# Kernel optimization log

Hardware: AMD Instinct MI355X
Metric: run time of the kernel (lower is better)

Reference implementation:

```python
import jax, jax.numpy as jnp
import numpy as np

H = 8          # num_heads
NB = 2         # block_num
EPS = 1e-8     # LayerNorm eps
NEG = -1e9


def layer_norm(x, g, b):
    m = jnp.mean(x, axis=-1, keepdims=True)
    v = jnp.var(x, axis=-1, keepdims=True)
    return (x - m) / jnp.sqrt(v + EPS) * g + b


def setup_inputs() -> dict:
    key = jax.random.key(0)
    B, L, D = 128, 200, 512
    ks = jax.random.split(key, 24)
    s = 0.02
    inp = {
        'log_seqs': jax.random.randint(ks[0], (B, L), 0, 50),
        'seqs_embs': jax.random.normal(ks[1], (B, L, D), jnp.float32),
        'entire_log_seqs': jax.random.randint(ks[2], (B, L), 0, 50),
        'Wq': jax.random.normal(ks[3], (NB, D, D), jnp.float32) * s,
        'bq': jnp.zeros((NB, D), jnp.float32),
        'Wk': jax.random.normal(ks[4], (NB, D, D), jnp.float32) * s,
        'bk': jnp.zeros((NB, D), jnp.float32),
        'Wv': jax.random.normal(ks[5], (NB, D, D), jnp.float32) * s,
        'bv': jnp.zeros((NB, D), jnp.float32),
        'ln_attn_g': jnp.ones((NB, D), jnp.float32),
        'ln_attn_b': jnp.zeros((NB, D), jnp.float32),
        'ln_fwd_g': jnp.ones((NB, D), jnp.float32),
        'ln_fwd_b': jnp.zeros((NB, D), jnp.float32),
        'W1': jax.random.normal(ks[6], (NB, D, D), jnp.float32) * s,
        'b1': jnp.zeros((NB, D), jnp.float32),
        'W2': jax.random.normal(ks[7], (NB, D, D), jnp.float32) * s,
        'b2': jnp.zeros((NB, D), jnp.float32),
        'ln_last_g': jnp.ones((D,), jnp.float32),
        'ln_last_b': jnp.zeros((D,), jnp.float32),
    }
    return inp


def reference(log_seqs, seqs_embs, entire_log_seqs,
              Wq, bq, Wk, bk, Wv, bv,
              ln_attn_g, ln_attn_b, ln_fwd_g, ln_fwd_b,
              W1, b1, W2, b2, ln_last_g, ln_last_b):
    B, L, D = seqs_embs.shape
    dk = D // H
    scale = 1.0 / np.sqrt(dk).astype(np.float32)

    tl_mask = (log_seqs == 0)            # [B,L] True at target-domain padding (source positions)
    all_mask = (entire_log_seqs != 0)    # [B,L]
    causal = jnp.tril(jnp.ones((L, L), bool))
    # attention_mask = tril * timeline_mask(keys) * all_timeline_mask(keys)
    attn_mask = causal[None, :, :] & tl_mask[:, None, :] & all_mask[:, None, :]  # [B,L,L]
    mf = attn_mask.astype(seqs_embs.dtype)

    keep = (~tl_mask)[..., None].astype(seqs_embs.dtype)  # target positions
    target = seqs_embs * keep
    source = seqs_embs * tl_mask[..., None].astype(seqs_embs.dtype)

    for i in range(NB):
        Qn = layer_norm(target, ln_attn_g[i], ln_attn_b[i])
        q = (Qn @ Wq[i] + bq[i]).reshape(B, L, H, dk).transpose(0, 2, 1, 3)
        k = (source @ Wk[i] + bk[i]).reshape(B, L, H, dk).transpose(0, 2, 1, 3)
        v = (source @ Wv[i] + bv[i]).reshape(B, L, H, dk).transpose(0, 2, 1, 3)
        scores = jnp.einsum('bhqd,bhkd->bhqk', q, k) * scale
        scores = jnp.where(attn_mask[:, None], scores, NEG)
        p = jax.nn.softmax(scores, axis=-1) * mf[:, None]   # double masking
        x = jnp.einsum('bhqk,bhkd->bhqd', p, v)
        x = x.transpose(0, 2, 1, 3).reshape(B, L, D)
        target = x if i == 0 else target + x
        target = layer_norm(target, ln_fwd_g[i], ln_fwd_b[i])
        # PointWiseFeedForward (1x1 convs == per-position linears) + residual
        h = jax.nn.relu(target @ W1[i] + b1[i])
        target = target + (h @ W2[i] + b2[i])
        target = target * keep

    out = layer_norm(target, ln_last_g, ln_last_b) * keep
    return out
```

## Files before the change

### kernel.cpp

```cpp
#include <hip/hip_runtime.h>
#include <hip/hip_bf16.h>

#define BB 128
#define LL 200
#define DD 512
#define HH 8
#define DK 64
#define NBLK 2
#define BL (BB*LL)
#define SCAP 64

typedef unsigned short ushort_t;
typedef unsigned int uint_t;
typedef __attribute__((ext_vector_type(8))) short short8;
typedef __attribute__((ext_vector_type(4))) short short4v;
typedef __attribute__((ext_vector_type(4))) float f32x4;

__device__ inline ushort_t f2b(float x) {
    unsigned u = __float_as_uint(x);
    unsigned r = (u + 0x7FFF + ((u >> 16) & 1)) >> 16;
    return (ushort_t)r;
}

__device__ inline float b2f(ushort_t u) {
    return __uint_as_float((uint_t)u << 16);
}

__device__ inline void gload16(const void* g, void* l) {
    __builtin_amdgcn_global_load_lds((const __attribute__((address_space(1))) void*)g,
                                     (__attribute__((address_space(3))) void*)l,
                                     16, 0, 0);
}

__global__ __launch_bounds__(256) void maskidx_kernel(const int* __restrict__ logs,
                                                      const int* __restrict__ entire,
                                                      float* __restrict__ keepf,
                                                      float* __restrict__ kmf,
                                                      int* __restrict__ kidx,
                                                      int* __restrict__ cntb) {
    int b = blockIdx.x;
    int t = threadIdx.x;
    bool valid = false;
    if (t < LL) {
        int i = b * LL + t;
        bool src = (logs[i] == 0);
        keepf[i] = src ? 0.f : 1.f;
        bool v = src && (entire[i] != 0);
        kmf[i] = v ? 1.f : 0.f;
        valid = v;
    }
    unsigned long long mask = __ballot(valid);
    int wid = t >> 6, lane = t & 63;
    __shared__ int wcnt[4];
    if (lane == 0) wcnt[wid] = __popcll(mask);
    __syncthreads();
    int base = 0;
    for (int k2 = 0; k2 < wid; k2++) base += wcnt[k2];
    int pos = base + __popcll(mask & ((1ull << lane) - 1ull));
    if (valid) kidx[b * LL + pos] = t;
    if (t == 0) cntb[b] = wcnt[0] + wcnt[1] + wcnt[2] + wcnt[3];
}

__global__ __launch_bounds__(128) void scan_kernel(const int* __restrict__ cntb,
                                                   const int* __restrict__ kidx,
                                                   int* __restrict__ off,
                                                   int* __restrict__ rows,
                                                   int* __restrict__ nbk) {
    __shared__ int soff[BB + 1];
    int t = threadIdx.x;
    if (t == 0) {
        int acc = 0;
        for (int b = 0; b < BB; b++) { soff[b] = acc; acc += cntb[b]; }
        soff[BB] = acc;
        nbk[0] = (acc + 127) >> 7;
    }
    __syncthreads();
    int ob = soff[t], nc = cntb[t];
    off[t] = ob;
    for (int s = 0; s < nc; s++)
        rows[ob + s] = t * LL + kidx[t * LL + s];
    __syncthreads();
    if (t == 0) {
        int S = soff[BB];
        int Spad = ((S + 127) >> 7) << 7;
        int last = (S > 0) ? rows[S - 1] : 0;
        for (int s = S; s < Spad; s++) rows[s] = last;
    }
}

__global__ __launch_bounds__(256) void prep_kernel(const int* __restrict__ logs,
                                                   const float* __restrict__ emb,
                                                   float* __restrict__ tgt,
                                                   ushort_t* __restrict__ srcb) {
    int row = blockIdx.x;
    int t = threadIdx.x;
    bool src = (logs[row] == 0);
    float kf = src ? 0.f : 1.f, sf = src ? 1.f : 0.f;
    size_t base = (size_t)row * DD;
    float e0 = emb[base + t], e1 = emb[base + t + 256];
    tgt[base + t] = e0 * kf;
    tgt[base + t + 256] = e1 * kf;
    srcb[base + t] = f2b(e0 * sf);
    srcb[base + t + 256] = f2b(e1 * sf);
}

__global__ __launch_bounds__(256) void wtrans10_kernel(const float* __restrict__ Wq,
                                                       const float* __restrict__ Wk,
                                                       const float* __restrict__ Wv,
                                                       const float* __restrict__ W1,
                                                       const float* __restrict__ W2,
                                                       ushort_t* __restrict__ WqkvT,
                                                       ushort_t* __restrict__ W1T,
                                                       ushort_t* __restrict__ W2T) {
    __shared__ float ts[32][33];
    int tx = threadIdx.x & 31, ty = threadIdx.x >> 5;
    int bx = blockIdx.x * 32, by = blockIdx.y * 32;
    int z = blockIdx.z;
    const float* Wm;
    ushort_t* Wtm;
    if (z < 6) {
        int i = z / 3, j = z - 3 * i;
        const float* src = (j == 0) ? Wq : (j == 1) ? Wk : Wv;
        Wm = src + (size_t)i * DD * DD;
        Wtm = WqkvT + (size_t)z * DD * DD;
    } else if (z < 8) {
        Wm = W1 + (size_t)(z - 6) * DD * DD;
        Wtm = W1T + (size_t)(z - 6) * DD * DD;
    } else {
        Wm = W2 + (size_t)(z - 8) * DD * DD;
        Wtm = W2T + (size_t)(z - 8) * DD * DD;
    }
    #pragma unroll
    for (int i = 0; i < 4; i++) {
        int r = ty + i * 8;
        ts[r][tx] = Wm[(size_t)(by + r) * DD + bx + tx];
    }
    __syncthreads();
    #pragma unroll
    for (int i = 0; i < 4; i++) {
        int r = ty + i * 8;
        Wtm[(size_t)(bx + r) * DD + by + tx] = f2b(ts[tx][r]);
    }
}

__global__ __launch_bounds__(256) void ln_kernel(const float* __restrict__ x,
                                                 const float* __restrict__ addx,
                                                 float* __restrict__ outf,
                                                 ushort_t* __restrict__ outb,
                                                 const float* __restrict__ g,
                                                 const float* __restrict__ bt,
                                                 const float* __restrict__ keepf) {
    int wid = threadIdx.x >> 6, lane = threadIdx.x & 63;
    int row = blockIdx.x * 4 + wid;
    size_t base = (size_t)row * DD;
    int c0 = lane * 4, c1 = c0 + 256;
    f32x4 v0 = *(const f32x4*)(x + base + c0);
    f32x4 v1 = *(const f32x4*)(x + base + c1);
    if (addx) {
        f32x4 a0 = *(const f32x4*)(addx + base + c0);
        f32x4 a1 = *(const f32x4*)(addx + base + c1);
        v0 = v0 + a0;
        v1 = v1 + a1;
    }
    float s = v0[0] + v0[1] + v0[2] + v0[3] + v1[0] + v1[1] + v1[2] + v1[3];
    float sq = v0[0] * v0[0] + v0[1] * v0[1] + v0[2] * v0[2] + v0[3] * v0[3]
             + v1[0] * v1[0] + v1[1] * v1[1] + v1[2] * v1[2] + v1[3] * v1[3];
    #pragma unroll
    for (int off = 32; off; off >>= 1) {
        s += __shfl_xor(s, off);
        sq += __shfl_xor(sq, off);
    }
    float mean = s * (1.f / DD);
    float var = sq * (1.f / DD) - mean * mean;
    float rstd = rsqrtf(fmaxf(var, 0.f) + 1e-8f);
    float kf = keepf ? keepf[row] : 1.f;
    f32x4 g0 = *(const f32x4*)(g + c0), g1 = *(const f32x4*)(g + c1);
    f32x4 b0 = *(const f32x4*)(bt + c0), b1 = *(const f32x4*)(bt + c1);
    f32x4 o0, o1;
    #pragma unroll
    for (int j = 0; j < 4; j++) {
        o0[j] = ((v0[j] - mean) * rstd * g0[j] + b0[j]) * kf;
        o1[j] = ((v1[j] - mean) * rstd * g1[j] + b1[j]) * kf;
    }
    if (outf) {
        *(f32x4*)(outf + base + c0) = o0;
        *(f32x4*)(outf + base + c1) = o1;
    }
    if (outb) {
        short4v ob0, ob1;
        #pragma unroll
        for (int j = 0; j < 4; j++) { ob0[j] = (short)f2b(o0[j]); ob1[j] = (short)f2b(o1[j]); }
        *(short4v*)(outb + base + c0) = ob0;
        *(short4v*)(outb + base + c1) = ob1;
    }
}

__global__ __launch_bounds__(256) void gemm_mfma(const ushort_t* __restrict__ A,
                                                 const ushort_t* __restrict__ Bt,
                                                 const float* __restrict__ bias,
                                                 float* __restrict__ Cf,
                                                 ushort_t* __restrict__ Cb,
                                                 const float* __restrict__ keepf,
                                                 int mode, int M, int N, int K) {
    __shared__ ushort_t smem[12288];
    ushort_t* sAm = smem;
    ushort_t* sBm = smem + 4096;
    int t = threadIdx.x;
    int w = t >> 6, lane = t & 63;
    int lr = lane & 15, lq = lane >> 4;

    int nwg = (M >> 6) * (N >> 7);
    int cpx = nwg >> 3;
    int swz = (blockIdx.x & 7) * cpx + (blockIdx.x >> 3);
    int m0 = (swz >> 2) * 64;
    int n0 = (swz & 3) * 128;

    f32x4 acc[4][2] = {};

    int eA = t * 8, rowA = eA >> 5, colA = eA & 31;

    for (int k0 = 0; k0 < K; k0 += 64) {
        #pragma unroll
        for (int hh = 0; hh < 2; hh++) {
            gload16(A + (size_t)(m0 + rowA) * K + k0 + hh * 32 + colA,
                    sAm + hh * 2048 + (w * 64) * 8);
            #pragma unroll
            for (int r = 0; r < 2; r++) {
                int e = (r * 256 + t) * 8;
                int row = e >> 5, col = e & 31;
                gload16(Bt + (size_t)(n0 + row) * K + k0 + hh * 32 + col,
                        sBm + hh * 4096 + (r * 256 + w * 64) * 8);
            }
        }
        __syncthreads();

        #pragma unroll
        for (int hh = 0; hh < 2; hh++) {
            short8 af[4], bf[2];
            #pragma unroll
            for (int mt = 0; mt < 4; mt++)
                af[mt] = *(const short8*)(sAm + hh * 2048 + (mt * 16 + lr) * 32 + lq * 8);
            #pragma unroll
            for (int nt = 0; nt < 2; nt++)
                bf[nt] = *(const short8*)(sBm + hh * 4096 + (w * 32 + nt * 16 + lr) * 32 + lq * 8);
            #pragma unroll
            for (int mt = 0; mt < 4; mt++)
                #pragma unroll
                for (int nt = 0; nt < 2; nt++)
                    acc[mt][nt] = __builtin_amdgcn_mfma_f32_16x16x32_bf16(af[mt], bf[nt], acc[mt][nt], 0, 0, 0);
        }
        __syncthreads();
    }

    if (mode != 2) {
        #pragma unroll
        for (int nt = 0; nt < 2; nt++) {
            int colL = w * 32 + nt * 16 + lr;
            float bv = bias[n0 + colL];
            #pragma unroll
            for (int mt = 0; mt < 4; mt++) {
                int rowL = mt * 16 + lq * 4;
                #pragma unroll
                for (int r = 0; r < 4; r++) {
                    float o = acc[mt][nt][r] + bv;
                    if (mode == 1) o = fmaxf(o, 0.f);
                    smem[(rowL + r) * 136 + colL] = f2b(o);
                }
            }
        }
        __syncthreads();
        int rr = t >> 2, cc = (t & 3) * 32;
        #pragma unroll
        for (int j = 0; j < 4; j++) {
            short8 vv = *(const short8*)(smem + rr * 136 + cc + j * 8);
            *(short8*)(Cb + (size_t)(m0 + rr) * N + n0 + cc + j * 8) = vv;
        }
    } else {
        float* sf = (float*)smem;
        #pragma unroll
        for (int half = 0; half < 2; half++) {
            #pragma unroll
            for (int nt = 0; nt < 2; nt++) {
                int colL = w * 32 + nt * 16 + lr;
                float bv = bias[n0 + colL];
                #pragma unroll
                for (int mt = half * 2; mt < half * 2 + 2; mt++) {
                    int rowL = mt * 16 + lq * 4 - half * 32;
                    #pragma unroll
                    for (int r = 0; r < 4; r++)
                        sf[(rowL + r) * 132 + colL] = acc[mt][nt][r] + bv;
                }
            }
            __syncthreads();
            int rr = t >> 3, cc = (t & 7) * 16;
            int grow = m0 + half * 32 + rr;
            float kf = keepf[grow];
            #pragma unroll
            for (int j = 0; j < 4; j++) {
                f32x4 oldv = *(const f32x4*)(Cf + (size_t)grow * N + n0 + cc + j * 4);
                f32x4 nv;
                #pragma unroll
                for (int x = 0; x < 4; x++)
                    nv[x] = (oldv[x] + sf[rr * 132 + cc + j * 4 + x]) * kf;
                *(f32x4*)(Cf + (size_t)grow * N + n0 + cc + j * 4) = nv;
            }
            __syncthreads();
        }
    }
}

__global__ __launch_bounds__(256) void gemm_kv(const ushort_t* __restrict__ A,
                                               const ushort_t* __restrict__ Bqkv,
                                               const float* __restrict__ bk,
                                               const float* __restrict__ bv,
                                               const int* __restrict__ rows,
                                               const int* __restrict__ nbk,
                                               ushort_t* __restrict__ kc,
                                               ushort_t* __restrict__ vc) {
    __shared__ ushort_t sA[2][128 * 32];
    __shared__ ushort_t sB[2][128 * 32];
    int z = blockIdx.z;
    const ushort_t* Bt = Bqkv + (size_t)(1 + z) * DD * DD;
    const float* bias = z ? bv : bk;
    ushort_t* C = z ? vc : kc;

    int t = threadIdx.x;
    int w = t >> 6, lane = t & 63;
    int wm = w & 1, wn = w >> 1;
    int n0 = blockIdx.y * 128;
    int lr = lane & 15, lq = lane >> 4;
    int colA = (t & 3) * 8;
    int nb = nbk[0];

    for (int mb = blockIdx.x; mb < nb; mb += gridDim.x) {
        int m0 = mb * 128;
        int ra0 = rows[m0 + (t >> 2)];
        int ra1 = rows[m0 + 64 + (t >> 2)];

        f32x4 acc[4][4] = {};

        for (int k0 = 0; k0 < DD; k0 += 64) {
            #pragma unroll
            for (int hh = 0; hh < 2; hh++) {
                gload16(A + (size_t)ra0 * DD + k0 + hh * 32 + colA,
                        sA[hh] + (0 * 256 + w * 64) * 8);
                gload16(A + (size_t)ra1 * DD + k0 + hh * 32 + colA,
                        sA[hh] + (1 * 256 + w * 64) * 8);
                #pragma unroll
                for (int r = 0; r < 2; r++) {
                    int e = (r * 256 + t) * 8;
                    int row = e >> 5, col = e & 31;
                    gload16(Bt + (size_t)(n0 + row) * DD + k0 + hh * 32 + col,
                            sB[hh] + (r * 256 + w * 64) * 8);
                }
            }
            __syncthreads();

            #pragma unroll
            for (int hh = 0; hh < 2; hh++) {
                short8 af[4], bf[4];
                #pragma unroll
                for (int mt = 0; mt < 4; mt++)
                    af[mt] = *(const short8*)(sA[hh] + (wm * 64 + mt * 16 + lr) * 32 + lq * 8);
                #pragma unroll
                for (int nt = 0; nt < 4; nt++)
                    bf[nt] = *(const short8*)(sB[hh] + (wn * 64 + nt * 16 + lr) * 32 + lq * 8);
                #pragma unroll
                for (int mt = 0; mt < 4; mt++)
                    #pragma unroll
                    for (int nt = 0; nt < 4; nt++)
                        acc[mt][nt] = __builtin_amdgcn_mfma_f32_16x16x32_bf16(af[mt], bf[nt], acc[mt][nt], 0, 0, 0);
            }
            __syncthreads();
        }

        #pragma unroll
        for (int nt = 0; nt < 4; nt++) {
            int col = n0 + wn * 64 + nt * 16 + lr;
            float bv2 = bias[col];
            #pragma unroll
            for (int mt = 0; mt < 4; mt++) {
                int rowb = m0 + wm * 64 + mt * 16 + lq * 4;
                #pragma unroll
                for (int r = 0; r < 4; r++)
                    C[(size_t)(rowb + r) * DD + col] = f2b(acc[mt][nt][r] + bv2);
            }
        }
    }
}

__global__ __launch_bounds__(256) void attn_sparse(const ushort_t* __restrict__ q,
                                                   const ushort_t* __restrict__ kc,
                                                   const ushort_t* __restrict__ vc,
                                                   const int* __restrict__ kidx,
                                                   const int* __restrict__ cntb,
                                                   const int* __restrict__ off,
                                                   float* __restrict__ xout) {
    __shared__ ushort_t sK[SCAP * DK];
    __shared__ ushort_t sV[SCAP * DK];
    __shared__ int sIdx[LL];
    int b = blockIdx.x >> 3, h = blockIdx.x & 7;
    int t = threadIdx.x;
    int w = t >> 6, lane = t & 63;
    int qi = lane >> 3;
    int dc = (lane & 7) * 8;
    int nc = cntb[b], ob = off[b];
    const ushort_t* qg = q + (size_t)b * LL * DD + h * DK;
    float* og = xout + (size_t)b * LL * DD + h * DK;
    const ushort_t* kb2 = kc + (size_t)ob * DD + h * DK;
    const ushort_t* vb2 = vc + (size_t)ob * DD + h * DK;

    if (t < nc) sIdx[t] = kidx[b * LL + t];
    int ns = (nc < SCAP) ? nc : SCAP;
    for (int idx = t; idx < ns * 8; idx += 256) {
        int s = idx >> 3, c = (idx & 7) * 8;
        *(uint4*)(sK + s * DK + c) = *(const uint4*)(kb2 + (size_t)s * DD + c);
        *(uint4*)(sV + s * DK + c) = *(const uint4*)(vb2 + (size_t)s * DD + c);
    }
    __syncthreads();

    for (int i0 = 0; i0 < LL; i0 += 32) {
        int i = i0 + w * 8 + qi;
        bool qok = (i < LL);
        int ic = qok ? i : (LL - 1);
        short8 qv = *(const short8*)(qg + (size_t)ic * DD + dc);
        float qf[8];
        #pragma unroll
        for (int j = 0; j < 8; j++) qf[j] = b2f((ushort_t)qv[j]);

        float m = -3.0e38f, l = 0.f;
        float acc[8];
        #pragma unroll
        for (int j = 0; j < 8; j++) acc[j] = 0.f;

        for (int s = 0; s < nc; s++) {
            const ushort_t* kp = (s < SCAP) ? (sK + s * DK + dc)
                                            : (kb2 + (size_t)s * DD + dc);
            const ushort_t* vp = (s < SCAP) ? (sV + s * DK + dc)
                                            : (vb2 + (size_t)s * DD + dc);
            short8 k8 = *(const short8*)kp;
            float pp = 0.f;
            #pragma unroll
            for (int j = 0; j < 8; j++) pp += qf[j] * b2f((ushort_t)k8[j]);
            pp += __shfl_xor(pp, 1);
            pp += __shfl_xor(pp, 2);
            pp += __shfl_xor(pp, 4);
            bool ok = (sIdx[s] <= i);
            float sc = ok ? pp * 0.125f : -3.0e38f;
            float mn = fmaxf(m, sc);
            float e = ok ? __expf(sc - mn) : 0.f;
            float rs2 = __expf(m - mn);
            l = l * rs2 + e;
            short8 v8 = *(const short8*)vp;
            #pragma unroll
            for (int j = 0; j < 8; j++)
                acc[j] = acc[j] * rs2 + e * b2f((ushort_t)v8[j]);
            m = mn;
        }

        if (qok) {
            float inv = (l > 0.f) ? 1.f / l : 0.f;
            f32x4 o0, o1;
            #pragma unroll
            for (int j = 0; j < 4; j++) { o0[j] = acc[j] * inv; o1[j] = acc[j + 4] * inv; }
            *(f32x4*)(og + (size_t)i * DD + dc) = o0;
            *(f32x4*)(og + (size_t)i * DD + dc + 4) = o1;
        }
    }
}

extern "C" void kernel_launch(void* const* d_in, const int* in_sizes, int n_in,
                              void* d_out, int out_size, void* d_ws, size_t ws_size,
                              hipStream_t stream) {
    const int* log_seqs = (const int*)d_in[0];
    const float* seqs_embs = (const float*)d_in[1];
    const int* entire = (const int*)d_in[2];
    const float* Wq = (const float*)d_in[3];
    const float* bq = (const float*)d_in[4];
    const float* Wk = (const float*)d_in[5];
    const float* bk = (const float*)d_in[6];
    const float* Wv = (const float*)d_in[7];
    const float* bv = (const float*)d_in[8];
    const float* lag = (const float*)d_in[9];
    const float* lab = (const float*)d_in[10];
    const float* lfg = (const float*)d_in[11];
    const float* lfb = (const float*)d_in[12];
    const float* W1 = (const float*)d_in[13];
    const float* b1 = (const float*)d_in[14];
    const float* W2 = (const float*)d_in[15];
    const float* b2 = (const float*)d_in[16];
    const float* llg = (const float*)d_in[17];
    const float* llb = (const float*)d_in[18];
    float* out = (float*)d_out;
    float* ws = (float*)d_ws;

    const size_t n = (size_t)BL * DD;
    float* tgt = ws;
    float* aout = ws + n;
    ushort_t* srcb = (ushort_t*)(ws + 2 * n);
    ushort_t* qb = srcb + n;
    ushort_t* kc = qb + n;
    ushort_t* lnb = kc + n;
    ushort_t* WqkvT = lnb + n;
    ushort_t* W1T = WqkvT + (size_t)NBLK * 3 * DD * DD;
    ushort_t* W2T = W1T + (size_t)NBLK * DD * DD;
    float* keepf = (float*)(W2T + (size_t)NBLK * DD * DD);
    float* kmf = keepf + BL;
    ushort_t* vc = (ushort_t*)(kmf + BL);
    int* kidx = (int*)(vc + n);
    int* cntb = kidx + BL;
    int* offb = cntb + BB;
    int* rows = offb + BB;
    int* nbk = rows + BL + 128;
    ushort_t* hb = qb;

    maskidx_kernel<<<BB, 256, 0, stream>>>(log_seqs, entire, keepf, kmf, kidx, cntb);
    scan_kernel<<<1, 128, 0, stream>>>(cntb, kidx, offb, rows, nbk);
    prep_kernel<<<BL, 256, 0, stream>>>(log_seqs, seqs_embs, tgt, srcb);
    dim3 tw(16, 16, 10);
    wtrans10_kernel<<<tw, 256, 0, stream>>>(Wq, Wk, Wv, W1, W2, WqkvT, W1T, W2T);

    int ngg = (BL / 64) * (DD / 128);
    int nln = BL / 4;
    dim3 gkv(32, DD / 128, 2);
    for (int i = 0; i < NBLK; i++) {
        size_t wo = (size_t)i * DD * DD;
        gemm_kv<<<gkv, 256, 0, stream>>>(srcb, WqkvT + (size_t)i * 3 * DD * DD,
                                         bk + i * DD, bv + i * DD, rows, nbk, kc, vc);
        ln_kernel<<<nln, 256, 0, stream>>>(tgt, nullptr, nullptr, lnb,
                                           lag + i * DD, lab + i * DD, nullptr);
        gemm_mfma<<<ngg, 256, 0, stream>>>(lnb, WqkvT + (size_t)i * 3 * DD * DD,
                                           bq + i * DD, nullptr, qb, nullptr,
                                           0, BL, DD, DD);
        attn_sparse<<<BB * HH, 256, 0, stream>>>(qb, kc, vc, kidx, cntb, offb, aout);
        ln_kernel<<<nln, 256, 0, stream>>>(aout, (i == 0) ? nullptr : tgt, tgt, lnb,
                                           lfg + i * DD, lfb + i * DD, nullptr);
        gemm_mfma<<<ngg, 256, 0, stream>>>(lnb, W1T + wo, b1 + i * DD, nullptr, hb,
                                           nullptr, 1, BL, DD, DD);
        gemm_mfma<<<ngg, 256, 0, stream>>>(hb, W2T + wo, b2 + i * DD, tgt, nullptr,
                                           keepf, 2, BL, DD, DD);
    }
    ln_kernel<<<nln, 256, 0, stream>>>(tgt, nullptr, out, nullptr, llg, llb, keepf);
}
```

Measured before the change: 531.6 us.

## Merge sparse K/V projection into Q GEMM launch and vectorize prep kernel

The separate gather-based K/V GEMM kernel is removed. Its work is now done by 64 extra workgroups appended to the Q-projection GEMM launch, each looping over 64-row tiles of the compacted source rows with the same 64x128 tile code. This removes one launch per block and lets the K/V work overlap the Q GEMM, but changes the K/V tile shape from 128x128 to 64x128 and limits that part to 64 workgroups, which could become the tail. Separately, the prep kernel now handles four rows per block with vector loads and stores.

```diff
diff --git a/kernel.cpp b/kernel.cpp
--- a/kernel.cpp
+++ b/kernel.cpp
@@ -92,16 +92,27 @@
                                                    const float* __restrict__ emb,
                                                    float* __restrict__ tgt,
                                                    ushort_t* __restrict__ srcb) {
-    int row = blockIdx.x;
-    int t = threadIdx.x;
+    int wid = threadIdx.x >> 6, lane = threadIdx.x & 63;
+    int row = blockIdx.x * 4 + wid;
     bool src = (logs[row] == 0);
     float kf = src ? 0.f : 1.f, sf = src ? 1.f : 0.f;
     size_t base = (size_t)row * DD;
-    float e0 = emb[base + t], e1 = emb[base + t + 256];
-    tgt[base + t] = e0 * kf;
-    tgt[base + t + 256] = e1 * kf;
-    srcb[base + t] = f2b(e0 * sf);
-    srcb[base + t + 256] = f2b(e1 * sf);
+    int c0 = lane * 4, c1 = c0 + 256;
+    f32x4 e0 = *(const f32x4*)(emb + base + c0);
+    f32x4 e1 = *(const f32x4*)(emb + base + c1);
+    f32x4 t0, t1;
+    short4v s0, s1;
+    #pragma unroll
+    for (int j = 0; j < 4; j++) {
+        t0[j] = e0[j] * kf;
+        t1[j] = e1[j] * kf;
+        s0[j] = (short)f2b(e0[j] * sf);
+        s1[j] = (short)f2b(e1[j] * sf);
+    }
+    *(f32x4*)(tgt + base + c0) = t0;
+    *(f32x4*)(tgt + base + c1) = t1;
+    *(short4v*)(srcb + base + c0) = s0;
+    *(short4v*)(srcb + base + c1) = s1;
 }
 
 __global__ __launch_bounds__(256) void wtrans10_kernel(const float* __restrict__ Wq,
@@ -201,190 +212,188 @@
                                                  float* __restrict__ Cf,
                                                  ushort_t* __restrict__ Cb,
                                                  const float* __restrict__ keepf,
-                                                 int mode, int M, int N, int K) {
+                                                 int mode, int M, int N, int K, int ngg,
+                                                 const ushort_t* __restrict__ Akv,
+                                                 const ushort_t* __restrict__ Bkv,
+                                                 const float* __restrict__ bk,
+                                                 const float* __restrict__ bv,
+                                                 const int* __restrict__ rows,
+                                                 const int* __restrict__ nbk,
+                                                 ushort_t* __restrict__ kc,
+                                                 ushort_t* __restrict__ vc) {
     __shared__ ushort_t smem[12288];
     ushort_t* sAm = smem;
     ushort_t* sBm = smem + 4096;
     int t = threadIdx.x;
     int w = t >> 6, lane = t & 63;
     int lr = lane & 15, lq = lane >> 4;
-
-    int nwg = (M >> 6) * (N >> 7);
-    int cpx = nwg >> 3;
-    int swz = (blockIdx.x & 7) * cpx + (blockIdx.x >> 3);
-    int m0 = (swz >> 2) * 64;
-    int n0 = (swz & 3) * 128;
-
-    f32x4 acc[4][2] = {};
-
     int eA = t * 8, rowA = eA >> 5, colA = eA & 31;
 
-    for (int k0 = 0; k0 < K; k0 += 64) {
-        #pragma unroll
-        for (int hh = 0; hh < 2; hh++) {
-            gload16(A + (size_t)(m0 + rowA) * K + k0 + hh * 32 + colA,
-                    sAm + hh * 2048 + (w * 64) * 8);
-            #pragma unroll
-            for (int r = 0; r < 2; r++) {
-                int e = (r * 256 + t) * 8;
-                int row = e >> 5, col = e & 31;
-                gload16(Bt + (size_t)(n0 + row) * K + k0 + hh * 32 + col,
-                        sBm + hh * 4096 + (r * 256 + w * 64) * 8);
-            }
-        }
-        __syncthreads();
-
-        #pragma unroll
-        for (int hh = 0; hh < 2; hh++) {
-            short8 af[4], bf[2];
-            #pragma unroll
-            for (int mt = 0; mt < 4; mt++)
-                af[mt] = *(const short8*)(sAm + hh * 2048 + (mt * 16 + lr) * 32 + lq * 8);
-            #pragma unroll
-            for (int nt = 0; nt < 2; nt++)
-                bf[nt] = *(const short8*)(sBm + hh * 4096 + (w * 32 + nt * 16 + lr) * 32 + lq * 8);
-            #pragma unroll
-            for (int mt = 0; mt < 4; mt++)
-                #pragma unroll
-                for (int nt = 0; nt < 2; nt++)
-                    acc[mt][nt] = __builtin_amdgcn_mfma_f32_16x16x32_bf16(af[mt], bf[nt], acc[mt][nt], 0, 0, 0);
-        }
-        __syncthreads();
-    }
-
-    if (mode != 2) {
-        #pragma unroll
-        for (int nt = 0; nt < 2; nt++) {
-            int colL = w * 32 + nt * 16 + lr;
-            float bv = bias[n0 + colL];
-            #pragma unroll
-            for (int mt = 0; mt < 4; mt++) {
-                int rowL = mt * 16 + lq * 4;
-                #pragma unroll
-                for (int r = 0; r < 4; r++) {
-                    float o = acc[mt][nt][r] + bv;
-                    if (mode == 1) o = fmaxf(o, 0.f);
-                    smem[(rowL + r) * 136 + colL] = f2b(o);
-                }
-            }
-        }
-        __syncthreads();
-        int rr = t >> 2, cc = (t & 3) * 32;
-        #pragma unroll
-        for (int j = 0; j < 4; j++) {
-            short8 vv = *(const short8*)(smem + rr * 136 + cc + j * 8);
-            *(short8*)(Cb + (size_t)(m0 + rr) * N + n0 + cc + j * 8) = vv;
-        }
-    } else {
-        float* sf = (float*)smem;
-        #pragma unroll
-        for (int half = 0; half < 2; half++) {
-            #pragma unroll
-            for (int nt = 0; nt < 2; nt++) {
-                int colL = w * 32 + nt * 16 + lr;
-                float bv = bias[n0 + colL];
-                #pragma unroll
-                for (int mt = half * 2; mt < half * 2 + 2; mt++) {
-                    int rowL = mt * 16 + lq * 4 - half * 32;
-                    #pragma unroll
-                    for (int r = 0; r < 4; r++)
-                        sf[(rowL + r) * 132 + colL] = acc[mt][nt][r] + bv;
-                }
-            }
-            __syncthreads();
-            int rr = t >> 3, cc = (t & 7) * 16;
-            int grow = m0 + half * 32 + rr;
-            float kf = keepf[grow];
-            #pragma unroll
-            for (int j = 0; j < 4; j++) {
-                f32x4 oldv = *(const f32x4*)(Cf + (size_t)grow * N + n0 + cc + j * 4);
-                f32x4 nv;
-                #pragma unroll
-                for (int x = 0; x < 4; x++)
-                    nv[x] = (oldv[x] + sf[rr * 132 + cc + j * 4 + x]) * kf;
-                *(f32x4*)(Cf + (size_t)grow * N + n0 + cc + j * 4) = nv;
-            }
-            __syncthreads();
-        }
-    }
-}
-
-__global__ __launch_bounds__(256) void gemm_kv(const ushort_t* __restrict__ A,
-                                               const ushort_t* __restrict__ Bqkv,
-                                               const float* __restrict__ bk,
-                                               const float* __restrict__ bv,
-                                               const int* __restrict__ rows,
-                                               const int* __restrict__ nbk,
-                                               ushort_t* __restrict__ kc,
-                                               ushort_t* __restrict__ vc) {
-    __shared__ ushort_t sA[2][128 * 32];
-    __shared__ ushort_t sB[2][128 * 32];
-    int z = blockIdx.z;
-    const ushort_t* Bt = Bqkv + (size_t)(1 + z) * DD * DD;
-    const float* bias = z ? bv : bk;
-    ushort_t* C = z ? vc : kc;
-
-    int t = threadIdx.x;
-    int w = t >> 6, lane = t & 63;
-    int wm = w & 1, wn = w >> 1;
-    int n0 = blockIdx.y * 128;
-    int lr = lane & 15, lq = lane >> 4;
-    int colA = (t & 3) * 8;
-    int nb = nbk[0];
-
-    for (int mb = blockIdx.x; mb < nb; mb += gridDim.x) {
-        int m0 = mb * 128;
-        int ra0 = rows[m0 + (t >> 2)];
-        int ra1 = rows[m0 + 64 + (t >> 2)];
-
-        f32x4 acc[4][4] = {};
-
-        for (int k0 = 0; k0 < DD; k0 += 64) {
+    if ((int)blockIdx.x < ngg) {
+        int cpx = ngg >> 3;
+        int swz = (blockIdx.x & 7) * cpx + (blockIdx.x >> 3);
+        int m0 = (swz >> 2) * 64;
+        int n0 = (swz & 3) * 128;
+
+        f32x4 acc[4][2] = {};
+
+        for (int k0 = 0; k0 < K; k0 += 64) {
             #pragma unroll
             for (int hh = 0; hh < 2; hh++) {
-                gload16(A + (size_t)ra0 * DD + k0 + hh * 32 + colA,
-                        sA[hh] + (0 * 256 + w * 64) * 8);
-                gload16(A + (size_t)ra1 * DD + k0 + hh * 32 + colA,
-                        sA[hh] + (1 * 256 + w * 64) * 8);
+                gload16(A + (size_t)(m0 + rowA) * K + k0 + hh * 32 + colA,
+                        sAm + hh * 2048 + (w * 64) * 8);
                 #pragma unroll
                 for (int r = 0; r < 2; r++) {
                     int e = (r * 256 + t) * 8;
                     int row = e >> 5, col = e & 31;
-                    gload16(Bt + (size_t)(n0 + row) * DD + k0 + hh * 32 + col,
-                            sB[hh] + (r * 256 + w * 64) * 8);
+                    gload16(Bt + (size_t)(n0 + row) * K + k0 + hh * 32 + col,
+                            sBm + hh * 4096 + (r * 256 + w * 64) * 8);
                 }
             }
             __syncthreads();
 
             #pragma unroll
             for (int hh = 0; hh < 2; hh++) {
-                short8 af[4], bf[4];
+                short8 af[4], bf[2];
                 #pragma unroll
                 for (int mt = 0; mt < 4; mt++)
-                    af[mt] = *(const short8*)(sA[hh] + (wm * 64 + mt * 16 + lr) * 32 + lq * 8);
-                #pragma unroll
-                for (int nt = 0; nt < 4; nt++)
-                    bf[nt] = *(const short8*)(sB[hh] + (wn * 64 + nt * 16 + lr) * 32 + lq * 8);
+                    af[mt] = *(const short8*)(sAm + hh * 2048 + (mt * 16 + lr) * 32 + lq * 8);
+                #pragma unroll
+                for (int nt = 0; nt < 2; nt++)
+                    bf[nt] = *(const short8*)(sBm + hh * 4096 + (w * 32 + nt * 16 + lr) * 32 + lq * 8);
                 #pragma unroll
                 for (int mt = 0; mt < 4; mt++)
                     #pragma unroll
-                    for (int nt = 0; nt < 4; nt++)
+                    for (int nt = 0; nt < 2; nt++)
                         acc[mt][nt] = __builtin_amdgcn_mfma_f32_16x16x32_bf16(af[mt], bf[nt], acc[mt][nt], 0, 0, 0);
             }
             __syncthreads();
         }
 
-        #pragma unroll
-        for (int nt = 0; nt < 4; nt++) {
-            int col = n0 + wn * 64 + nt * 16 + lr;
-            float bv2 = bias[col];
-            #pragma unroll
-            for (int mt = 0; mt < 4; mt++) {
-                int rowb = m0 + wm * 64 + mt * 16 + lq * 4;
-                #pragma unroll
-                for (int r = 0; r < 4; r++)
-                    C[(size_t)(rowb + r) * DD + col] = f2b(acc[mt][nt][r] + bv2);
-            }
+        if (mode != 2) {
+            #pragma unroll
+            for (int nt = 0; nt < 2; nt++) {
+                int colL = w * 32 + nt * 16 + lr;
+                float bvv = bias[n0 + colL];
+                #pragma unroll
+                for (int mt = 0; mt < 4; mt++) {
+                    int rowL = mt * 16 + lq * 4;
+                    #pragma unroll
+                    for (int r = 0; r < 4; r++) {
+                        float o = acc[mt][nt][r] + bvv;
+                        if (mode == 1) o = fmaxf(o, 0.f);
+                        smem[(rowL + r) * 136 + colL] = f2b(o);
+                    }
+                }
+            }
+            __syncthreads();
+            int rr = t >> 2, cc = (t & 3) * 32;
+            #pragma unroll
+            for (int j = 0; j < 4; j++) {
+                short8 vv = *(const short8*)(smem + rr * 136 + cc + j * 8);
+                *(short8*)(Cb + (size_t)(m0 + rr) * N + n0 + cc + j * 8) = vv;
+            }
+        } else {
+            float* sf = (float*)smem;
+            #pragma unroll
+            for (int half = 0; half < 2; half++) {
+                #pragma unroll
+                for (int nt = 0; nt < 2; nt++) {
+                    int colL = w * 32 + nt * 16 + lr;
+                    float bvv = bias[n0 + colL];
+                    #pragma unroll
+                    for (int mt = half * 2; mt < half * 2 + 2; mt++) {
+                        int rowL = mt * 16 + lq * 4 - half * 32;
+                        #pragma unroll
+                        for (int r = 0; r < 4; r++)
+                            sf[(rowL + r) * 132 + colL] = acc[mt][nt][r] + bvv;
+                    }
+                }
+                __syncthreads();
+                int rr = t >> 3, cc = (t & 7) * 16;
+                int grow = m0 + half * 32 + rr;
+                float kf = keepf[grow];
+                #pragma unroll
+                for (int j = 0; j < 4; j++) {
+                    f32x4 oldv = *(const f32x4*)(Cf + (size_t)grow * N + n0 + cc + j * 4);
+                    f32x4 nv;
+                    #pragma unroll
+                    for (int x = 0; x < 4; x++)
+                        nv[x] = (oldv[x] + sf[rr * 132 + cc + j * 4 + x]) * kf;
+                    *(f32x4*)(Cf + (size_t)grow * N + n0 + cc + j * 4) = nv;
+                }
+                __syncthreads();
+            }
+        }
+    } else {
+        int eb = blockIdx.x - ngg;
+        int z = eb >> 5;
+        int n0 = ((eb >> 3) & 3) * 128;
+        int mt0 = eb & 7;
+        const ushort_t* Btk = Bkv + (size_t)z * DD * DD;
+        const float* biask = z ? bv : bk;
+        ushort_t* C = z ? vc : kc;
+        int rowlim = nbk[0] * 128;
+
+        for (int mt = mt0; mt * 64 < rowlim; mt += 8) {
+            int m0c = mt * 64;
+            int ra = rows[m0c + rowA];
+
+            f32x4 acc[4][2] = {};
+
+            for (int k0 = 0; k0 < DD; k0 += 64) {
+                #pragma unroll
+                for (int hh = 0; hh < 2; hh++) {
+                    gload16(Akv + (size_t)ra * DD + k0 + hh * 32 + colA,
+                            sAm + hh * 2048 + (w * 64) * 8);
+                    #pragma unroll
+                    for (int r = 0; r < 2; r++) {
+                        int e = (r * 256 + t) * 8;
+                        int row = e >> 5, col = e & 31;
+                        gload16(Btk + (size_t)(n0 + row) * DD + k0 + hh * 32 + col,
+                                sBm + hh * 4096 + (r * 256 + w * 64) * 8);
+                    }
+                }
+                __syncthreads();
+
+                #pragma unroll
+                for (int hh = 0; hh < 2; hh++) {
+                    short8 af[4], bf[2];
+                    #pragma unroll
+                    for (int mt2 = 0; mt2 < 4; mt2++)
+                        af[mt2] = *(const short8*)(sAm + hh * 2048 + (mt2 * 16 + lr) * 32 + lq * 8);
+                    #pragma unroll
+                    for (int nt = 0; nt < 2; nt++)
+                        bf[nt] = *(const short8*)(sBm + hh * 4096 + (w * 32 + nt * 16 + lr) * 32 + lq * 8);
+                    #pragma unroll
+                    for (int mt2 = 0; mt2 < 4; mt2++)
+                        #pragma unroll
+                        for (int nt = 0; nt < 2; nt++)
+                            acc[mt2][nt] = __builtin_amdgcn_mfma_f32_16x16x32_bf16(af[mt2], bf[nt], acc[mt2][nt], 0, 0, 0);
+                }
+                __syncthreads();
+            }
+
+            #pragma unroll
+            for (int nt = 0; nt < 2; nt++) {
+                int colL = w * 32 + nt * 16 + lr;
+                float bvv = biask[n0 + colL];
+                #pragma unroll
+                for (int mt2 = 0; mt2 < 4; mt2++) {
+                    int rowL = mt2 * 16 + lq * 4;
+                    #pragma unroll
+                    for (int r = 0; r < 4; r++)
+                        smem[(rowL + r) * 136 + colL] = f2b(acc[mt2][nt][r] + bvv);
+                }
+            }
+            __syncthreads();
+            int rr = t >> 2, cc = (t & 3) * 32;
+            #pragma unroll
+            for (int j = 0; j < 4; j++) {
+                short8 vv = *(const short8*)(smem + rr * 136 + cc + j * 8);
+                *(short8*)(C + (size_t)(m0c + rr) * DD + n0 + cc + j * 8) = vv;
+            }
+            __syncthreads();
         }
     }
 }
@@ -516,29 +525,33 @@
 
     maskidx_kernel<<<BB, 256, 0, stream>>>(log_seqs, entire, keepf, kmf, kidx, cntb);
     scan_kernel<<<1, 128, 0, stream>>>(cntb, kidx, offb, rows, nbk);
-    prep_kernel<<<BL, 256, 0, stream>>>(log_seqs, seqs_embs, tgt, srcb);
+    prep_kernel<<<BL / 4, 256, 0, stream>>>(log_seqs, seqs_embs, tgt, srcb);
     dim3 tw(16, 16, 10);
     wtrans10_kernel<<<tw, 256, 0, stream>>>(Wq, Wk, Wv, W1, W2, WqkvT, W1T, W2T);
 
     int ngg = (BL / 64) * (DD / 128);
     int nln = BL / 4;
-    dim3 gkv(32, DD / 128, 2);
     for (int i = 0; i < NBLK; i++) {
         size_t wo = (size_t)i * DD * DD;
-        gemm_kv<<<gkv, 256, 0, stream>>>(srcb, WqkvT + (size_t)i * 3 * DD * DD,
-                                         bk + i * DD, bv + i * DD, rows, nbk, kc, vc);
+        const ushort_t* Wi = WqkvT + (size_t)i * 3 * DD * DD;
         ln_kernel<<<nln, 256, 0, stream>>>(tgt, nullptr, nullptr, lnb,
                                            lag + i * DD, lab + i * DD, nullptr);
-        gemm_mfma<<<ngg, 256, 0, stream>>>(lnb, WqkvT + (size_t)i * 3 * DD * DD,
-                                           bq + i * DD, nullptr, qb, nullptr,
-                                           0, BL, DD, DD);
+        gemm_mfma<<<ngg + 64, 256, 0, stream>>>(lnb, Wi, bq + i * DD, nullptr, qb,
+                                                nullptr, 0, BL, DD, DD, ngg,
+                                                srcb, Wi + (size_t)DD * DD,
+                                                bk + i * DD, bv + i * DD,
+                                                rows, nbk, kc, vc);
         attn_sparse<<<BB * HH, 256, 0, stream>>>(qb, kc, vc, kidx, cntb, offb, aout);
         ln_kernel<<<nln, 256, 0, stream>>>(aout, (i == 0) ? nullptr : tgt, tgt, lnb,
                                            lfg + i * DD, lfb + i * DD, nullptr);
         gemm_mfma<<<ngg, 256, 0, stream>>>(lnb, W1T + wo, b1 + i * DD, nullptr, hb,
-                                           nullptr, 1, BL, DD, DD);
+                                           nullptr, 1, BL, DD, DD, ngg,
+                                           nullptr, nullptr, nullptr, nullptr,
+                                           nullptr, nullptr, nullptr, nullptr);
         gemm_mfma<<<ngg, 256, 0, stream>>>(hb, W2T + wo, b2 + i * DD, tgt, nullptr,
-                                           keepf, 2, BL, DD, DD);
+                                           keepf, 2, BL, DD, DD, ngg,
+                                           nullptr, nullptr, nullptr, nullptr,
+                                           nullptr, nullptr, nullptr, nullptr);
     }
     ln_kernel<<<nln, 256, 0, stream>>>(tgt, nullptr, out, nullptr, llg, llb, keepf);
 }
```

After: 503.2 us. -5.4%, faster.
